# Optimization experiments

Hardware: AMD Instinct MI355X
Metric: run time of the kernel (lower is better)

The kernel has to match this reference:

```python
import jax, jax.numpy as jnp
import numpy as np

B, V, N, IN_F, HEADS, OUT_F = 4, 4, 1000, 64, 4, 32
D = HEADS * OUT_F  # 128, concat=True
E = 64000
NEG_SLOPE = 0.2


def setup_inputs() -> dict:
    key = jax.random.key(0)
    ks = jax.random.split(key, 8)
    x = jax.random.normal(ks[0], (B, V, N, IN_F), jnp.float32)
    edge_index = jax.random.randint(ks[1], (2, E), 0, B * N, dtype=jnp.int64)
    W = jax.random.normal(ks[2], (HEADS * OUT_F, IN_F), jnp.float32) / np.sqrt(IN_F)
    att = jax.random.normal(ks[3], (1, HEADS, 2 * OUT_F), jnp.float32) * 0.1
    in_proj_w = jax.random.normal(ks[4], (3 * D, D), jnp.float32) / np.sqrt(D)
    in_proj_b = jnp.zeros((3 * D,), jnp.float32)
    out_proj_w = jax.random.normal(ks[5], (D, D), jnp.float32) / np.sqrt(D)
    out_proj_b = jnp.zeros((D,), jnp.float32)
    bias = jnp.zeros((D,), jnp.float32)
    return dict(x=x, W=W, att=att, in_proj_w=in_proj_w, in_proj_b=in_proj_b,
                out_proj_w=out_proj_w, out_proj_b=out_proj_b, bias=bias,
                edge_index=edge_index)


def reference(x, W, att, in_proj_w, in_proj_b, out_proj_w, out_proj_b, bias, edge_index):
    Bx, Vx, Nx, _ = x.shape
    Ntot = Bx * Nx
    # intra-view GAT: shared W across views
    h = jnp.einsum('bvni,oi->bvno', x, W).reshape(Bx, Vx, Nx, HEADS, OUT_F)
    # block-diagonal placement: h_full[b*V+v, b*N:(b+1)*N] = h[b,v]
    ib = jnp.arange(Bx)
    hf = jnp.zeros((Bx, Vx, Bx, Nx, HEADS, OUT_F), x.dtype).at[ib, :, ib].set(h)
    h_full = hf.reshape(Bx * Vx, Ntot, HEADS, OUT_F)
    # add self loops
    loops = jnp.arange(Ntot, dtype=edge_index.dtype)
    src = jnp.concatenate([edge_index[0], loops])
    dst = jnp.concatenate([edge_index[1], loops])
    # attention scores (faithful to source: flatten h_full over (B*V, Ntot) and
    # index with raw node ids, i.e. gathers from block 0 only)
    h_flat = h_full.reshape(Bx * Vx * Ntot, HEADS, OUT_F)
    h_cat = jnp.concatenate([h_flat[src], h_flat[dst]], axis=-1)  # [Etot, H, 2*OUT]
    att_in = jax.nn.leaky_relu(h_cat, NEG_SLOPE)
    scores = jnp.sum(att * att_in, axis=-1)  # [Etot, HEADS]
    # per-destination segment softmax
    seg_max = jax.ops.segment_max(scores, dst, num_segments=Ntot)
    seg_max = jax.lax.stop_gradient(jnp.where(jnp.isfinite(seg_max), seg_max, 0.0))
    ex = jnp.exp(scores - seg_max[dst])
    denom = jax.ops.segment_sum(ex, dst, num_segments=Ntot)
    alpha = ex / (denom[dst] + 1e-16)  # [Etot, HEADS]
    # scatter-add aggregation, broadcast over B*V rows
    msgs = h_full[:, src] * alpha[None, :, :, None]  # [B*V, Etot, H, OUT]
    out_full = jnp.zeros_like(h_full).at[:, dst].add(msgs)
    # extract each graph's own node block
    out = out_full.reshape(Bx, Vx, Bx, Nx, HEADS, OUT_F)[ib, :, ib]  # [B,V,N,H,OUT]
    h_gat = out.reshape(Bx, Vx, Nx, HEADS * OUT_F)  # concat heads
    # inter-view mixing: MHA over the V axis per node
    seq = h_gat.transpose(0, 2, 1, 3).reshape(Bx * Nx, Vx, D)
    q, k, v = jnp.split(seq @ in_proj_w.T + in_proj_b, 3, axis=-1)
    hd = D // HEADS
    sp = lambda t: t.reshape(Bx * Nx, Vx, HEADS, hd).transpose(0, 2, 1, 3)
    q, k, v = sp(q), sp(k), sp(v)
    aw = jax.nn.softmax(jnp.einsum('bhqd,bhkd->bhqk', q, k) / jnp.sqrt(jnp.asarray(hd, x.dtype)), axis=-1)
    ao = jnp.einsum('bhqk,bhkd->bhqd', aw, v).transpose(0, 2, 1, 3).reshape(Bx * Nx, Vx, D)
    mixed = ao @ out_proj_w.T + out_proj_b
    h_mixed = mixed.reshape(Bx, Nx, Vx, D).transpose(0, 2, 1, 3)  # [B,V,N,D]
    return h_mixed + bias
```

## Files before the change

### kernel.cpp

```cpp
#include <hip/hip_runtime.h>

#define NN 1000
#define HEADS_ 4
#define DM 128
#define EE 64000
#define NTOT 4000
#define ETOT 68000
#define CAP 48
#define EB 34
#define QS 388

template <int KK, int SCORE>
__device__ void gemm64(int mi, int ni,
                       const float* __restrict__ A, const float* __restrict__ Wt,
                       float* __restrict__ C, int N,
                       const float* __restrict__ att,
                       float* __restrict__ ssrc, float* __restrict__ sdst) {
  __shared__ float As[64 * 64];
  __shared__ float Bs[64 * 64];
  int tid = threadIdx.x;
  int m0 = mi * 64, n0 = ni * 64;
  int tx = tid & 15, ty = tid >> 4;
  const float4* A4 = (const float4*)A;
  const float4* W4 = (const float4*)Wt;
  float acc[4][4] = {};

  for (int c = 0; c < KK / 64; ++c) {
    __syncthreads();
    {
      int q = tid & 15, r0 = tid >> 4;
#pragma unroll
      for (int p = 0; p < 4; ++p) {
        int r = r0 + p * 16;
        float4 v = A4[(size_t)(m0 + r) * (KK / 4) + c * 16 + q];
        *(float4*)&As[r * 64 + ((q ^ ((r >> 2) & 15)) << 2)] = v;
      }
#pragma unroll
      for (int p = 0; p < 4; ++p) {
        int r = r0 + p * 16;
        float4 v = W4[(size_t)(n0 + r) * (KK / 4) + c * 16 + q];
        *(float4*)&Bs[r * 64 + ((q ^ ((r >> 2) & 15)) << 2)] = v;
      }
    }
    __syncthreads();
#pragma unroll 4
    for (int q = 0; q < 16; ++q) {
      float4 a[4], b[4];
      int sa = (q ^ ty) << 2;
      int sb = (q ^ tx) << 2;
#pragma unroll
      for (int i = 0; i < 4; ++i)
        a[i] = *(const float4*)&As[(ty * 4 + i) * 64 + sa];
#pragma unroll
      for (int j = 0; j < 4; ++j)
        b[j] = *(const float4*)&Bs[(tx * 4 + j) * 64 + sb];
#pragma unroll
      for (int i = 0; i < 4; ++i)
#pragma unroll
        for (int j = 0; j < 4; ++j)
          acc[i][j] += a[i].x * b[j].x + a[i].y * b[j].y
                     + a[i].z * b[j].z + a[i].w * b[j].w;
    }
  }

  int nc = n0 + tx * 4;
#pragma unroll
  for (int i = 0; i < 4; ++i) {
    int m = m0 + ty * 4 + i;
    *(float4*)&C[(size_t)m * N + nc] =
        make_float4(acc[i][0], acc[i][1], acc[i][2], acc[i][3]);
  }

  if (SCORE && m0 < NN) {
    int hsel = tx >> 3;
    int h = ni * 2 + hsel;
    int kb = (tx & 7) * 4;
    float a0[4], a1[4];
#pragma unroll
    for (int j = 0; j < 4; ++j) {
      a0[j] = att[h * 64 + kb + j];
      a1[j] = att[h * 64 + 32 + kb + j];
    }
#pragma unroll
    for (int i = 0; i < 4; ++i) {
      int m = m0 + ty * 4 + i;
      float p0 = 0.f, p1 = 0.f;
#pragma unroll
      for (int j = 0; j < 4; ++j) {
        float g = acc[i][j];
        float lr = g > 0.f ? g : 0.2f * g;
        p0 += a0[j] * lr;
        p1 += a1[j] * lr;
      }
      p0 += __shfl_xor(p0, 1, 16); p1 += __shfl_xor(p1, 1, 16);
      p0 += __shfl_xor(p0, 2, 16); p1 += __shfl_xor(p1, 2, 16);
      p0 += __shfl_xor(p0, 4, 16); p1 += __shfl_xor(p1, 4, 16);
      if ((tx & 7) == 0 && m < NN) {
        ssrc[m * HEADS_ + h] = p0;
        sdst[m * HEADS_ + h] = p1;
      }
    }
  }
}

__global__ __launch_bounds__(256) void k1_kernel(const float* __restrict__ x,
                                                 const float* __restrict__ W,
                                                 const float* __restrict__ att,
                                                 float* __restrict__ hbuf,
                                                 float* __restrict__ ssrc,
                                                 float* __restrict__ sdst,
                                                 const int* __restrict__ ei,
                                                 int* __restrict__ cnt,
                                                 int* __restrict__ elist) {
  int bid = blockIdx.x;
  if (bid < 500) {
    gemm64<64, 1>(bid >> 1, bid & 1, x, W, hbuf, 128, att, ssrc, sdst);
  } else {
    for (int e = (bid - 500) * 256 + threadIdx.x; e < ETOT; e += EB * 256) {
      int s, d;
      if (e < EE) { s = ei[e]; d = ei[EE + e]; }
      else { s = d = e - EE; }
      int pos = atomicAdd(&cnt[d], 1);
      if (pos < CAP) elist[d * CAP + pos] = s;
    }
  }
}

__global__ __launch_bounds__(512) void mega_kernel(const int* __restrict__ cnt,
                                                   const int* __restrict__ elist,
                                                   const float* __restrict__ ssrc,
                                                   const float* __restrict__ sdst,
                                                   const float* __restrict__ hbuf,
                                                   const float* __restrict__ inw,
                                                   const float* __restrict__ inb,
                                                   const float* __restrict__ outw,
                                                   const float* __restrict__ outb,
                                                   const float* __restrict__ bias,
                                                   float* __restrict__ out) {
  extern __shared__ float smem[];
  float* As   = smem;
  float* rg2  = smem + 8448;
  float* exsF = rg2;
  int*   srcsI = (int*)(rg2 + 3072);
  float* Bs   = rg2 + 4096;
  float* qk   = rg2;
  float* ao   = rg2;
  float* Bs2  = rg2 + 8192;

  int tid = threadIdx.x;
  int g0n = blockIdx.x * 16;

  {
    int ln = tid >> 5, t32 = tid & 31;
    int d = g0n + ln;
    int m = cnt[d]; if (m > CAP) m = CAP;
    for (int base = 0; base < m; base += 8) {
      int i = base + (t32 >> 2);
      if (i < m) {
        int s = elist[d * CAP + i];
        if ((t32 & 3) == 0) srcsI[ln * CAP + i] = s;
        float sc = ssrc[s * HEADS_ + (t32 & 3)] + sdst[d * HEADS_ + (t32 & 3)];
        exsF[ln * 192 + i * 4 + (t32 & 3)] = __expf(sc);
      }
    }
  }
  __syncthreads();

  {
    int r = tid >> 3, g = tid & 7;
    int ln = r >> 2, v = r & 3;
    int d = g0n + ln, b = d / NN;
    int m = cnt[d]; if (m > CAP) m = CAP;
    const float* hbase = hbuf + ((size_t)(b * 4 + v) * NN) * DM + g * 4;
    float4 a0 = make_float4(0.f, 0.f, 0.f, 0.f), a1 = a0, a2 = a0, a3 = a0;
    float4 den = make_float4(1e-16f, 1e-16f, 1e-16f, 1e-16f);
    for (int i = 0; i < m; ++i) {
      float4 ex = *(const float4*)&exsF[ln * 192 + i * 4];
      unsigned sl = (unsigned)(srcsI[ln * CAP + i] - b * NN);
      unsigned sc = sl < NN ? sl : 0u;
      const float* hrow = hbase + (size_t)sc * DM;
      float4 h0 = *(const float4*)(hrow);
      float4 h1 = *(const float4*)(hrow + 32);
      float4 h2 = *(const float4*)(hrow + 64);
      float4 h3 = *(const float4*)(hrow + 96);
      den.x += ex.x; den.y += ex.y; den.z += ex.z; den.w += ex.w;
      float w0 = sl < NN ? ex.x : 0.f, w1 = sl < NN ? ex.y : 0.f;
      float w2 = sl < NN ? ex.z : 0.f, w3 = sl < NN ? ex.w : 0.f;
      a0.x += w0 * h0.x; a0.y += w0 * h0.y; a0.z += w0 * h0.z; a0.w += w0 * h0.w;
      a1.x += w1 * h1.x; a1.y += w1 * h1.y; a1.z += w1 * h1.z; a1.w += w1 * h1.w;
      a2.x += w2 * h2.x; a2.y += w2 * h2.y; a2.z += w2 * h2.z; a2.w += w2 * h2.w;
      a3.x += w3 * h3.x; a3.y += w3 * h3.y; a3.z += w3 * h3.z; a3.w += w3 * h3.w;
    }
    float i0 = 1.f / den.x, i1 = 1.f / den.y, i2 = 1.f / den.z, i3 = 1.f / den.w;
    *(float4*)&As[r * 132 +       g * 4] = make_float4(a0.x * i0, a0.y * i0, a0.z * i0, a0.w * i0);
    *(float4*)&As[r * 132 +  32 + g * 4] = make_float4(a1.x * i1, a1.y * i1, a1.z * i1, a1.w * i1);
    *(float4*)&As[r * 132 +  64 + g * 4] = make_float4(a2.x * i2, a2.y * i2, a2.z * i2, a2.w * i2);
    *(float4*)&As[r * 132 +  96 + g * 4] = make_float4(a3.x * i3, a3.y * i3, a3.z * i3, a3.w * i3);
  }

  int tx = tid & 31, ty = tid >> 5;
  float acc[3][4][4] = {};
  {
    const float4* W4 = (const float4*)inw;
#pragma unroll
    for (int c = 0; c < 2; ++c) {
#pragma unroll
      for (int ni = 0; ni < 3; ++ni) {
        __syncthreads();
        {
          int q = tid & 15, r0 = tid >> 4;
#pragma unroll
          for (int p = 0; p < 4; ++p) {
            int r = r0 + p * 32;
            float4 v = W4[(size_t)(ni * 128 + r) * 32 + c * 16 + q];
            *(float4*)&Bs[r * 64 + ((q ^ ((r >> 2) & 15)) << 2)] = v;
          }
        }
        __syncthreads();
#pragma unroll 4
        for (int q = 0; q < 16; ++q) {
          float4 a[4], b[4];
          int sb = (q ^ (tx & 15)) << 2;
#pragma unroll
          for (int i = 0; i < 4; ++i)
            a[i] = *(const float4*)&As[(ty * 4 + i) * 132 + c * 64 + q * 4];
#pragma unroll
          for (int j = 0; j < 4; ++j)
            b[j] = *(const float4*)&Bs[(tx * 4 + j) * 64 + sb];
#pragma unroll
          for (int i = 0; i < 4; ++i)
#pragma unroll
            for (int j = 0; j < 4; ++j)
              acc[ni][i][j] += a[i].x * b[j].x + a[i].y * b[j].y
                             + a[i].z * b[j].z + a[i].w * b[j].w;
        }
      }
    }
  }
  __syncthreads();

#pragma unroll
  for (int ni = 0; ni < 3; ++ni) {
    int nc = ni * 128 + tx * 4;
    float4 bb = *(const float4*)&inb[nc];
#pragma unroll
    for (int i = 0; i < 4; ++i) {
      int r = ty * 4 + i;
      *(float4*)&qk[r * QS + nc] =
          make_float4(acc[ni][i][0] + bb.x, acc[ni][i][1] + bb.y,
                      acc[ni][i][2] + bb.z, acc[ni][i][3] + bb.w);
    }
  }
  __syncthreads();

  int ln = tid >> 5;
  int vq2 = (tid >> 3) & 3, h2 = (tid >> 1) & 3, s2 = tid & 1;
  float aww[4];
  {
    const float* qr = &qk[(ln * 4 + vq2) * QS + h2 * 32 + s2 * 16];
    float4 qv[4];
#pragma unroll
    for (int u = 0; u < 4; ++u) qv[u] = *(const float4*)&qr[u * 4];
    float sc[4];
#pragma unroll
    for (int vk = 0; vk < 4; ++vk) {
      const float* kr = &qk[(ln * 4 + vk) * QS + 128 + h2 * 32 + s2 * 16];
      float s = 0.f;
#pragma unroll
      for (int u = 0; u < 4; ++u) {
        float4 kv = *(const float4*)&kr[u * 4];
        s += qv[u].x * kv.x + qv[u].y * kv.y + qv[u].z * kv.z + qv[u].w * kv.w;
      }
      sc[vk] = s;
    }
#pragma unroll
    for (int vk = 0; vk < 4; ++vk)
      sc[vk] = (sc[vk] + __shfl_xor(sc[vk], 1)) * 0.17677669529663687f;
    float mx = fmaxf(fmaxf(sc[0], sc[1]), fmaxf(sc[2], sc[3]));
    float e0 = __expf(sc[0] - mx), e1 = __expf(sc[1] - mx);
    float e2 = __expf(sc[2] - mx), e3 = __expf(sc[3] - mx);
    float inv = 1.f / (e0 + e1 + e2 + e3);
    aww[0] = e0 * inv; aww[1] = e1 * inv; aww[2] = e2 * inv; aww[3] = e3 * inv;
  }

  float4 o[4];
#pragma unroll
  for (int u = 0; u < 4; ++u) o[u] = make_float4(0.f, 0.f, 0.f, 0.f);
#pragma unroll
  for (int vk = 0; vk < 4; ++vk) {
    const float* vr = &qk[(ln * 4 + vk) * QS + 256 + h2 * 32 + s2 * 16];
    float w = aww[vk];
#pragma unroll
    for (int u = 0; u < 4; ++u) {
      float4 vv = *(const float4*)&vr[u * 4];
      o[u].x += w * vv.x; o[u].y += w * vv.y;
      o[u].z += w * vv.z; o[u].w += w * vv.w;
    }
  }
  __syncthreads();
  {
    int r = ln * 4 + vq2;
#pragma unroll
    for (int u = 0; u < 4; ++u) {
      int qp = h2 * 8 + s2 * 4 + u;
      int cc = qp >> 4, qg = qp & 15;
      *(float4*)&ao[cc * 4096 + r * 64 + ((qg ^ (ln & 15)) << 2)] = o[u];
    }
  }
  __syncthreads();

  float oc[4][4] = {};
  const float4* O4 = (const float4*)outw;
#pragma unroll
  for (int c = 0; c < 2; ++c) {
    {
      int q = tid & 15, r0 = tid >> 4;
#pragma unroll
      for (int p = 0; p < 4; ++p) {
        int r = r0 + p * 32;
        float4 v = O4[(size_t)r * 32 + c * 16 + q];
        *(float4*)&Bs2[r * 64 + ((q ^ ((r >> 2) & 15)) << 2)] = v;
      }
    }
    __syncthreads();
#pragma unroll 4
    for (int q = 0; q < 16; ++q) {
      float4 a[4], bq[4];
      int sa = (q ^ ty) << 2;
      int sb = (q ^ (tx & 15)) << 2;
#pragma unroll
      for (int i = 0; i < 4; ++i)
        a[i] = *(const float4*)&ao[c * 4096 + (ty * 4 + i) * 64 + sa];
#pragma unroll
      for (int j = 0; j < 4; ++j)
        bq[j] = *(const float4*)&Bs2[(tx * 4 + j) * 64 + sb];
#pragma unroll
      for (int i = 0; i < 4; ++i)
#pragma unroll
        for (int j = 0; j < 4; ++j)
          oc[i][j] += a[i].x * bq[j].x + a[i].y * bq[j].y
                    + a[i].z * bq[j].z + a[i].w * bq[j].w;
    }
    __syncthreads();
  }

  {
    int nc = tx * 4;
    float4 ob = make_float4(outb[nc] + bias[nc], outb[nc + 1] + bias[nc + 1],
                            outb[nc + 2] + bias[nc + 2], outb[nc + 3] + bias[nc + 3]);
#pragma unroll
    for (int i = 0; i < 4; ++i) {
      int r = ty * 4 + i;
      int node = g0n + (r >> 2), vv = r & 3;
      int bg = node / NN, n = node - bg * NN;
      int om = (bg * 4 + vv) * NN + n;
      *(float4*)&out[(size_t)om * DM + nc] =
          make_float4(oc[i][0] + ob.x, oc[i][1] + ob.y,
                      oc[i][2] + ob.z, oc[i][3] + ob.w);
    }
  }
}

extern "C" void kernel_launch(void* const* d_in, const int* in_sizes, int n_in,
                              void* d_out, int out_size, void* d_ws, size_t ws_size,
                              hipStream_t stream) {
  const float* x    = (const float*)d_in[0];
  const float* W    = (const float*)d_in[1];
  const float* att  = (const float*)d_in[2];
  const float* inw  = (const float*)d_in[3];
  const float* inb  = (const float*)d_in[4];
  const float* outw = (const float*)d_in[5];
  const float* outb = (const float*)d_in[6];
  const float* bias = (const float*)d_in[7];
  const int*   ei   = (const int*)d_in[8];
  float* out = (float*)d_out;

  float* ws = (float*)d_ws;
  float* hbuf  = ws;
  float* ssrc  = ws + 12500000;
  float* sdst  = ssrc + 16000;
  int*   cnt   = (int*)(sdst + 16000);
  int*   elist = cnt + 4000;

  static int lds_opt_in = 0;
  if (!lds_opt_in) {
    hipFuncSetAttribute((const void*)mega_kernel,
                        hipFuncAttributeMaxDynamicSharedMemorySize, 160 * 1024);
    lds_opt_in = 1;
  }

  hipMemsetAsync(ssrc, 0, 36000 * sizeof(float), stream);

  k1_kernel<<<500 + EB, 256, 0, stream>>>(x, W, att, hbuf, ssrc, sdst, ei, cnt, elist);
  mega_kernel<<<250, 512, 133120, stream>>>(cnt, elist, ssrc, sdst, hbuf,
                                            inw, inb, outw, outb, bias, out);
}
```

Measured before the change: 138.2 us.

## Halve nodes per block and compute view attention in registers via shuffles

The fused GAT+MHA kernel now handles 8 nodes per block with 256 threads and about 49 KB of static LDS instead of 16 nodes, 512 threads and 130 KB of dynamic LDS. This doubles the grid to 500 blocks and allows more blocks per CU. The q/k/v staging through shared memory is removed: the per-head QK scores are reduced across lanes with warp shuffles, and softmax and the V weighting run directly on the GEMM accumulators. Each block now reloads the in_proj and out_proj weights for half as many rows, which doubles total weight traffic.

Result: no change. 139.9 us (+1.2%).

```diff
diff --git a/kernel.cpp b/kernel.cpp
--- a/kernel.cpp
+++ b/kernel.cpp
@@ -8,7 +8,6 @@
 #define ETOT 68000
 #define CAP 48
 #define EB 34
-#define QS 388
 
 template <int KK, int SCORE>
 __device__ void gemm64(int mi, int ni,
@@ -126,29 +125,28 @@
   }
 }
 
-__global__ __launch_bounds__(512) void mega_kernel(const int* __restrict__ cnt,
-                                                   const int* __restrict__ elist,
-                                                   const float* __restrict__ ssrc,
-                                                   const float* __restrict__ sdst,
-                                                   const float* __restrict__ hbuf,
-                                                   const float* __restrict__ inw,
-                                                   const float* __restrict__ inb,
-                                                   const float* __restrict__ outw,
-                                                   const float* __restrict__ outb,
-                                                   const float* __restrict__ bias,
-                                                   float* __restrict__ out) {
-  extern __shared__ float smem[];
-  float* As   = smem;
-  float* rg2  = smem + 8448;
-  float* exsF = rg2;
-  int*   srcsI = (int*)(rg2 + 3072);
-  float* Bs   = rg2 + 4096;
-  float* qk   = rg2;
-  float* ao   = rg2;
-  float* Bs2  = rg2 + 8192;
+__global__ __launch_bounds__(256) void mega2_kernel(const int* __restrict__ cnt,
+                                                    const int* __restrict__ elist,
+                                                    const float* __restrict__ ssrc,
+                                                    const float* __restrict__ sdst,
+                                                    const float* __restrict__ hbuf,
+                                                    const float* __restrict__ inw,
+                                                    const float* __restrict__ inb,
+                                                    const float* __restrict__ outw,
+                                                    const float* __restrict__ outb,
+                                                    const float* __restrict__ bias,
+                                                    float* __restrict__ out) {
+  __shared__ float smem[12416];
+  float* As    = smem;
+  float* rg2   = smem + 4224;
+  float* exsF  = rg2;
+  int*   srcsI = (int*)(rg2 + 1536);
+  float* Bs    = rg2;
+  float* Bs2   = rg2;
+  float* aoS   = smem;
 
   int tid = threadIdx.x;
-  int g0n = blockIdx.x * 16;
+  int g0n = blockIdx.x * 8;
 
   {
     int ln = tid >> 5, t32 = tid & 31;
@@ -210,8 +208,8 @@
         {
           int q = tid & 15, r0 = tid >> 4;
 #pragma unroll
-          for (int p = 0; p < 4; ++p) {
-            int r = r0 + p * 32;
+          for (int p = 0; p < 8; ++p) {
+            int r = r0 + p * 16;
             float4 v = W4[(size_t)(ni * 128 + r) * 32 + c * 16 + q];
             *(float4*)&Bs[r * 64 + ((q ^ ((r >> 2) & 15)) << 2)] = v;
           }
@@ -237,77 +235,57 @@
       }
     }
   }
+
+#pragma unroll
+  for (int ni = 0; ni < 3; ++ni) {
+    float4 ib = *(const float4*)&inb[ni * 128 + tx * 4];
+#pragma unroll
+    for (int i = 0; i < 4; ++i) {
+      acc[ni][i][0] += ib.x; acc[ni][i][1] += ib.y;
+      acc[ni][i][2] += ib.z; acc[ni][i][3] += ib.w;
+    }
+  }
+  float S[4][4];
+#pragma unroll
+  for (int vq = 0; vq < 4; ++vq)
+#pragma unroll
+    for (int vk = 0; vk < 4; ++vk)
+      S[vq][vk] = acc[0][vq][0] * acc[1][vk][0] + acc[0][vq][1] * acc[1][vk][1]
+                + acc[0][vq][2] * acc[1][vk][2] + acc[0][vq][3] * acc[1][vk][3];
+#pragma unroll
+  for (int vq = 0; vq < 4; ++vq)
+#pragma unroll
+    for (int vk = 0; vk < 4; ++vk) {
+      float s = S[vq][vk];
+      s += __shfl_xor(s, 1);
+      s += __shfl_xor(s, 2);
+      s += __shfl_xor(s, 4);
+      S[vq][vk] = s * 0.17677669529663687f;
+    }
+#pragma unroll
+  for (int vq = 0; vq < 4; ++vq) {
+    float mx = fmaxf(fmaxf(S[vq][0], S[vq][1]), fmaxf(S[vq][2], S[vq][3]));
+    float e0 = __expf(S[vq][0] - mx), e1 = __expf(S[vq][1] - mx);
+    float e2 = __expf(S[vq][2] - mx), e3 = __expf(S[vq][3] - mx);
+    float inv = 1.f / (e0 + e1 + e2 + e3);
+    S[vq][0] = e0 * inv; S[vq][1] = e1 * inv; S[vq][2] = e2 * inv; S[vq][3] = e3 * inv;
+  }
+  float4 ao_r[4];
+#pragma unroll
+  for (int vq = 0; vq < 4; ++vq) {
+    ao_r[vq] = make_float4(
+        S[vq][0] * acc[2][0][0] + S[vq][1] * acc[2][1][0] + S[vq][2] * acc[2][2][0] + S[vq][3] * acc[2][3][0],
+        S[vq][0] * acc[2][0][1] + S[vq][1] * acc[2][1][1] + S[vq][2] * acc[2][2][1] + S[vq][3] * acc[2][3][1],
+        S[vq][0] * acc[2][0][2] + S[vq][1] * acc[2][1][2] + S[vq][2] * acc[2][2][2] + S[vq][3] * acc[2][3][2],
+        S[vq][0] * acc[2][0][3] + S[vq][1] * acc[2][1][3] + S[vq][2] * acc[2][2][3] + S[vq][3] * acc[2][3][3]);
+  }
   __syncthreads();
-
-#pragma unroll
-  for (int ni = 0; ni < 3; ++ni) {
-    int nc = ni * 128 + tx * 4;
-    float4 bb = *(const float4*)&inb[nc];
-#pragma unroll
-    for (int i = 0; i < 4; ++i) {
-      int r = ty * 4 + i;
-      *(float4*)&qk[r * QS + nc] =
-          make_float4(acc[ni][i][0] + bb.x, acc[ni][i][1] + bb.y,
-                      acc[ni][i][2] + bb.z, acc[ni][i][3] + bb.w);
-    }
-  }
-  __syncthreads();
-
-  int ln = tid >> 5;
-  int vq2 = (tid >> 3) & 3, h2 = (tid >> 1) & 3, s2 = tid & 1;
-  float aww[4];
-  {
-    const float* qr = &qk[(ln * 4 + vq2) * QS + h2 * 32 + s2 * 16];
-    float4 qv[4];
-#pragma unroll
-    for (int u = 0; u < 4; ++u) qv[u] = *(const float4*)&qr[u * 4];
-    float sc[4];
-#pragma unroll
-    for (int vk = 0; vk < 4; ++vk) {
-      const float* kr = &qk[(ln * 4 + vk) * QS + 128 + h2 * 32 + s2 * 16];
-      float s = 0.f;
-#pragma unroll
-      for (int u = 0; u < 4; ++u) {
-        float4 kv = *(const float4*)&kr[u * 4];
-        s += qv[u].x * kv.x + qv[u].y * kv.y + qv[u].z * kv.z + qv[u].w * kv.w;
-      }
-      sc[vk] = s;
-    }
-#pragma unroll
-    for (int vk = 0; vk < 4; ++vk)
-      sc[vk] = (sc[vk] + __shfl_xor(sc[vk], 1)) * 0.17677669529663687f;
-    float mx = fmaxf(fmaxf(sc[0], sc[1]), fmaxf(sc[2], sc[3]));
-    float e0 = __expf(sc[0] - mx), e1 = __expf(sc[1] - mx);
-    float e2 = __expf(sc[2] - mx), e3 = __expf(sc[3] - mx);
-    float inv = 1.f / (e0 + e1 + e2 + e3);
-    aww[0] = e0 * inv; aww[1] = e1 * inv; aww[2] = e2 * inv; aww[3] = e3 * inv;
-  }
-
-  float4 o[4];
-#pragma unroll
-  for (int u = 0; u < 4; ++u) o[u] = make_float4(0.f, 0.f, 0.f, 0.f);
-#pragma unroll
-  for (int vk = 0; vk < 4; ++vk) {
-    const float* vr = &qk[(ln * 4 + vk) * QS + 256 + h2 * 32 + s2 * 16];
-    float w = aww[vk];
-#pragma unroll
-    for (int u = 0; u < 4; ++u) {
-      float4 vv = *(const float4*)&vr[u * 4];
-      o[u].x += w * vv.x; o[u].y += w * vv.y;
-      o[u].z += w * vv.z; o[u].w += w * vv.w;
-    }
-  }
-  __syncthreads();
-  {
-    int r = ln * 4 + vq2;
-#pragma unroll
-    for (int u = 0; u < 4; ++u) {
-      int qp = h2 * 8 + s2 * 4 + u;
-      int cc = qp >> 4, qg = qp & 15;
-      *(float4*)&ao[cc * 4096 + r * 64 + ((qg ^ (ln & 15)) << 2)] = o[u];
-    }
-  }
-  __syncthreads();
+  {
+    int cc = tx >> 4, g = tx & 15;
+#pragma unroll
+    for (int vq = 0; vq < 4; ++vq)
+      *(float4*)&aoS[cc * 2048 + (ty * 4 + vq) * 64 + ((g ^ ty) << 2)] = ao_r[vq];
+  }
 
   float oc[4][4] = {};
   const float4* O4 = (const float4*)outw;
@@ -316,8 +294,8 @@
     {
       int q = tid & 15, r0 = tid >> 4;
 #pragma unroll
-      for (int p = 0; p < 4; ++p) {
-        int r = r0 + p * 32;
+      for (int p = 0; p < 8; ++p) {
+        int r = r0 + p * 16;
         float4 v = O4[(size_t)r * 32 + c * 16 + q];
         *(float4*)&Bs2[r * 64 + ((q ^ ((r >> 2) & 15)) << 2)] = v;
       }
@@ -330,7 +308,7 @@
       int sb = (q ^ (tx & 15)) << 2;
 #pragma unroll
       for (int i = 0; i < 4; ++i)
-        a[i] = *(const float4*)&ao[c * 4096 + (ty * 4 + i) * 64 + sa];
+        a[i] = *(const float4*)&aoS[c * 2048 + (ty * 4 + i) * 64 + sa];
 #pragma unroll
       for (int j = 0; j < 4; ++j)
         bq[j] = *(const float4*)&Bs2[(tx * 4 + j) * 64 + sb];
@@ -382,16 +360,9 @@
   int*   cnt   = (int*)(sdst + 16000);
   int*   elist = cnt + 4000;
 
-  static int lds_opt_in = 0;
-  if (!lds_opt_in) {
-    hipFuncSetAttribute((const void*)mega_kernel,
-                        hipFuncAttributeMaxDynamicSharedMemorySize, 160 * 1024);
-    lds_opt_in = 1;
-  }
-
   hipMemsetAsync(ssrc, 0, 36000 * sizeof(float), stream);
 
   k1_kernel<<<500 + EB, 256, 0, stream>>>(x, W, att, hbuf, ssrc, sdst, ei, cnt, elist);
-  mega_kernel<<<250, 512, 133120, stream>>>(cnt, elist, ssrc, sdst, hbuf,
-                                            inw, inb, outw, outb, bias, out);
+  mega2_kernel<<<NTOT / 8, 256, 0, stream>>>(cnt, elist, ssrc, sdst, hbuf,
+                                             inw, inb, outw, outb, bias, out);
 }
```
